# Kernel optimization log

Measured on AMD Instinct MI355X. Metric: run time of the kernel, lower is better.

The kernel has to match this reference:

```python
import jax, jax.numpy as jnp
import numpy as np

B, N, D, H = 4, 4096, 1024, 16
HD = D // H


def setup_inputs() -> dict:
    key = jax.random.key(0)
    k_x, k_qkv, k_proj, k_b = jax.random.split(key, 4)
    x = jax.random.normal(k_x, (B, N, D), dtype=jnp.float32)
    # torch nn.Linear weights: (out_features, in_features)
    w_qkv = jax.random.normal(k_qkv, (3 * D, D), dtype=jnp.float32) * (D ** -0.5)
    w_proj = jax.random.normal(k_proj, (D, D), dtype=jnp.float32) * (D ** -0.5)
    b_proj = jax.random.normal(k_b, (D,), dtype=jnp.float32) * 0.01
    return {"x": x, "w_qkv": w_qkv, "w_proj": w_proj, "b_proj": b_proj}


def reference(x, w_qkv, w_proj, b_proj):
    b, n, d = x.shape
    # qkv projection (no bias, qkv_bias=False)
    qkv = x @ w_qkv.T                       # (b, n, 3d)
    qkv = qkv.reshape(b, n, 3, H, HD)
    q, k, v = qkv[:, :, 0], qkv[:, :, 1], qkv[:, :, 2]   # each (b, n, H, HD)
    # Faithful to source: q @ k.transpose(-2,-1) with q,k of shape (b,n,H,HD)
    # -> per-token (H,H) attention across heads, softmax over last (head) axis.
    scale = HD ** -0.5
    attn = jnp.einsum('bnhd,bngd->bnhg', q, k) * scale   # (b, n, H, H)
    attn = jax.nn.softmax(attn, axis=-1)
    o = jnp.einsum('bnhg,bngd->bnhd', attn, v)           # (b, n, H, HD)
    # source: transpose(1,2).reshape(b,n,d) (contiguous copy then reshape)
    o = jnp.swapaxes(o, 1, 2).reshape(b, n, d)
    return o @ w_proj.T + b_proj
```

## Files before the change

### kernel.cpp

```cpp
#include <hip/hip_runtime.h>
#include <hip/hip_bf16.h>
#include <cstdint>
#include <cstddef>

#define NB      4
#define NSEQ    4096
#define DM      1024
#define NTOK    16384
#define QKV_N   3072
#define TPW     8

typedef __attribute__((ext_vector_type(8))) short short8_t;
typedef __attribute__((ext_vector_type(4))) short short4_t;
typedef __attribute__((ext_vector_type(4))) float f32x4;

static __device__ __forceinline__ unsigned short f2bf(float f) {
    unsigned u = __builtin_bit_cast(unsigned, f);
    u += 0x7fffu + ((u >> 16) & 1u);
    return (unsigned short)(u >> 16);
}

static __device__ __forceinline__ void async16(const void* g, void* l) {
    __builtin_amdgcn_global_load_lds(
        (const __attribute__((address_space(1))) void*)g,
        (__attribute__((address_space(3))) void*)l, 16, 0, 0);
}

__global__ void cvt_all(const float* __restrict__ x,
                        const float* __restrict__ wqkv,
                        const float* __restrict__ wproj,
                        unsigned short* __restrict__ xb,
                        unsigned short* __restrict__ wqkvb,
                        unsigned short* __restrict__ wprojb)
{
    const int stride = gridDim.x * blockDim.x;
    for (int i = blockIdx.x * blockDim.x + threadIdx.x; i < 5242880; i += stride) {
        const float* src; unsigned short* dst; int off;
        if (i < 4194304)      { src = x;     dst = xb;     off = i; }
        else if (i < 4980736) { src = wqkv;  dst = wqkvb;  off = i - 4194304; }
        else                  { src = wproj; dst = wprojb; off = i - 4980736; }
        float4 f = ((const float4*)src)[off];
        unsigned lo = (unsigned)f2bf(f.x) | ((unsigned)f2bf(f.y) << 16);
        unsigned hi = (unsigned)f2bf(f.z) | ((unsigned)f2bf(f.w) << 16);
        ((uint2*)dst)[off] = make_uint2(lo, hi);
    }
}

template <bool BF16_OUT, bool BIAS>
__global__ __launch_bounds__(512, 2)
void gemm256(const unsigned short* __restrict__ A,
             const unsigned short* __restrict__ Bm,
             void* __restrict__ Cv,
             const float* __restrict__ bias,
             int M, int N, int K)
{
    __shared__ alignas(16) unsigned short As[2][16384];
    __shared__ alignas(16) unsigned short Bs[2][16384];

    const int t    = threadIdx.x;
    const int lane = t & 63;
    const int wave = t >> 6;
    const int quad = lane >> 4;
    const int r16  = lane & 15;
    const int wm   = wave >> 2;
    const int wn   = wave & 3;

    const int nwg = gridDim.x;
    const int swz = (blockIdx.x & 7) * (nwg >> 3) + (blockIdx.x >> 3);
    const int ntn = N >> 8;
    const int tm  = swz / ntn, tn = swz - tm * ntn;
    const int m0  = tm << 8, n0 = tn << 8;

    const int srow = t >> 3;
    const int schk = ((t & 7) ^ (srow & 7)) << 3;
    const unsigned short* gA = A  + (size_t)(m0 + srow) * K + schk;
    const unsigned short* gB = Bm + (size_t)(n0 + srow) * K + schk;
    unsigned short* const lA = &As[0][0] + t * 8;
    unsigned short* const lB = &Bs[0][0] + t * 8;

    const int NT = K >> 6;

#define STA(buf, kt, r) async16(gA + (size_t)(r) * 64 * K + (size_t)(kt) * 64, \
                                lA + (buf) * 16384 + (r) * 4096)
#define STB(buf, kt, r) async16(gB + (size_t)(r) * 64 * K + (size_t)(kt) * 64, \
                                lB + (buf) * 16384 + (r) * 4096)

    const int cs0 = ((quad    ) ^ (r16 & 7)) << 3;
    const int cs1 = ((quad ^ 4) ^ (r16 & 7)) << 3;
    const int aRow = wm * 128 + r16;
    const int bRow = wn * 64  + r16;

    f32x4 acc[8][4] = {};

#define RD_A(QR) _Pragma("unroll") for (int ii = 0; ii < 4; ++ii) {            \
        a[ii][0] = *(const short8_t*)(Ab + (aRow + (QR)*64 + ii*16) * 64 + cs0); \
        a[ii][1] = *(const short8_t*)(Ab + (aRow + (QR)*64 + ii*16) * 64 + cs1); }
#define RD_B(bb, QC) _Pragma("unroll") for (int jj = 0; jj < 2; ++jj) {        \
        bb[jj][0] = *(const short8_t*)(Bb + (bRow + (QC)*32 + jj*16) * 64 + cs0); \
        bb[jj][1] = *(const short8_t*)(Bb + (bRow + (QC)*32 + jj*16) * 64 + cs1); }
#define MM(QR, QC, bb) _Pragma("unroll") for (int s = 0; s < 2; ++s)           \
      _Pragma("unroll") for (int ii = 0; ii < 4; ++ii)                          \
        _Pragma("unroll") for (int jj = 0; jj < 2; ++jj)                        \
          acc[(QR)*4+ii][(QC)*2+jj] = __builtin_amdgcn_mfma_f32_16x16x32_bf16( \
              a[ii][s], bb[jj][s], acc[(QR)*4+ii][(QC)*2+jj], 0, 0, 0);
#define SYNC_PRE  __builtin_amdgcn_s_barrier();                                \
                  asm volatile("s_waitcnt lgkmcnt(0)" ::: "memory");           \
                  __builtin_amdgcn_sched_barrier(0);                           \
                  __builtin_amdgcn_s_setprio(1);
#define SYNC_POST __builtin_amdgcn_s_setprio(0);                               \
                  __builtin_amdgcn_s_barrier();                                \
                  asm volatile("" ::: "memory");

    STA(0,0,0); STA(0,0,1); STA(0,0,2); STA(0,0,3);
    STB(0,0,0); STB(0,0,1); STB(0,0,2); STB(0,0,3);
    STA(1,1,0); STA(1,1,1); STA(1,1,2); STA(1,1,3);
    STB(1,1,0); STB(1,1,1); STB(1,1,2); STB(1,1,3);
    asm volatile("s_waitcnt vmcnt(8)" ::: "memory");
    __builtin_amdgcn_s_barrier();

    for (int g = 0; g < NT; ++g) {
        const int cur = g & 1;
        const unsigned short* Ab = &As[cur][0];
        const unsigned short* Bb = &Bs[cur][0];
        const bool pf = (g + 2 < NT);
        short8_t a[4][2], b0[2][2], b1[2][2];

        RD_A(0) RD_B(b0, 0)
        SYNC_PRE
        MM(0, 0, b0)
        SYNC_POST

        RD_B(b1, 1)
        if (pf) { STA(cur, g+2, 0); STA(cur, g+2, 2); }
        SYNC_PRE
        MM(0, 1, b1)
        SYNC_POST

        RD_A(1)
        if (pf) { STB(cur, g+2, 0); STB(cur, g+2, 1); }
        SYNC_PRE
        MM(1, 0, b0)
        SYNC_POST

        if (pf) { STA(cur, g+2, 1); STA(cur, g+2, 3);
                  STB(cur, g+2, 2); STB(cur, g+2, 3); }
        __builtin_amdgcn_s_barrier();
        __builtin_amdgcn_s_setprio(1);
        MM(1, 1, b1)
        __builtin_amdgcn_s_setprio(0);
        if (pf)              asm volatile("s_waitcnt vmcnt(8)" ::: "memory");
        else if (g + 1 < NT) asm volatile("s_waitcnt vmcnt(0)" ::: "memory");
        __builtin_amdgcn_s_barrier();
        asm volatile("" ::: "memory");
    }

#undef STA
#undef STB
#undef RD_A
#undef RD_B
#undef MM
#undef SYNC_PRE
#undef SYNC_POST

    #pragma unroll
    for (int ri = 0; ri < 8; ++ri) {
        const int row = m0 + wm * 128 + (ri >> 2) * 64 + (ri & 3) * 16 + quad * 4;
        #pragma unroll
        for (int cj = 0; cj < 4; ++cj) {
            const int col = n0 + wn * 64 + (cj >> 1) * 32 + (cj & 1) * 16 + r16;
            float bv = 0.f;
            if constexpr (BIAS) bv = bias[col];
            #pragma unroll
            for (int r = 0; r < 4; ++r) {
                float v = acc[ri][cj][r] + bv;
                if constexpr (BF16_OUT)
                    ((unsigned short*)Cv)[(size_t)(row + r) * N + col] = f2bf(v);
                else
                    ((float*)Cv)[(size_t)(row + r) * N + col] = v;
            }
        }
    }
}

__global__ __launch_bounds__(256)
void attn_kernel(const unsigned short* __restrict__ qkv,
                 unsigned short* __restrict__ operm)
{
    __shared__ alignas(16) unsigned short s_qkv[4][2][QKV_N];
    __shared__ alignas(16) unsigned short s_p[4][256];
    __shared__ alignas(16) unsigned short s_o[4][16 * 72];
    const int t     = threadIdx.x;
    const int lane  = t & 63;
    const int wave  = t >> 6;
    const int quad  = lane >> 4;
    const int r16   = lane & 15;
    const int tok0  = blockIdx.x * (4 * TPW) + wave * TPW;

    {
        const unsigned short* src = qkv + (size_t)tok0 * QKV_N;
        #pragma unroll
        for (int i = 0; i < 6; ++i)
            async16(src + i * 512 + lane * 8, &s_qkv[wave][0][i * 512 + lane * 8]);
    }

    #pragma unroll
    for (int it = 0; it < TPW; ++it) {
        const int buf   = it & 1;
        const int token = tok0 + it;

        if (it + 1 < TPW) {
            const unsigned short* src = qkv + (size_t)(token + 1) * QKV_N;
            #pragma unroll
            for (int i = 0; i < 6; ++i)
                async16(src + i * 512 + lane * 8,
                        &s_qkv[wave][buf ^ 1][i * 512 + lane * 8]);
        }
        if (it == 0)           { asm volatile("s_waitcnt vmcnt(6)" ::: "memory"); }
        else if (it + 1 < TPW) { asm volatile("s_waitcnt vmcnt(8)" ::: "memory"); }
        else                   { asm volatile("s_waitcnt vmcnt(2)" ::: "memory"); }
        __builtin_amdgcn_sched_barrier(0);

        const unsigned short* q  = &s_qkv[wave][buf][0];
        const unsigned short* kk = q + 1024;
        const unsigned short* vv = q + 2048;

        f32x4 s = {};
        #pragma unroll
        for (int c = 0; c < 64; c += 32) {
            short8_t aq = *(const short8_t*)(q  + r16 * 64 + c + quad * 8);
            short8_t bk = *(const short8_t*)(kk + r16 * 64 + c + quad * 8);
            s = __builtin_amdgcn_mfma_f32_16x16x32_bf16(aq, bk, s, 0, 0, 0);
        }

        #pragma unroll
        for (int r = 0; r < 4; ++r) {
            float x = s[r] * 0.125f;
            float m = x;
            #pragma unroll
            for (int o = 1; o < 16; o <<= 1) m = fmaxf(m, __shfl_xor(m, o));
            float e = __expf(x - m);
            float su = e;
            #pragma unroll
            for (int o = 1; o < 16; o <<= 1) su += __shfl_xor(su, o);
            s_p[wave][(quad * 4 + r) * 16 + r16] = f2bf(e * __builtin_amdgcn_rcpf(su));
        }

        f32x4 o[4];
#if __has_builtin(__builtin_amdgcn_mfma_f32_16x16x16bf16_1k)
        short4_t pa = *(const short4_t*)(&s_p[wave][r16 * 16 + quad * 4]);
        #pragma unroll
        for (int j = 0; j < 4; ++j) {
            short4_t vb;
            #pragma unroll
            for (int e = 0; e < 4; ++e)
                vb[e] = (short)vv[(quad * 4 + e) * 64 + j * 16 + r16];
            f32x4 z = {};
            o[j] = __builtin_amdgcn_mfma_f32_16x16x16bf16_1k(pa, vb, z, 0, 0, 0);
        }
#else
        short8_t pa = {};
        if (quad < 2) pa = *(const short8_t*)(&s_p[wave][r16 * 16 + quad * 8]);
        #pragma unroll
        for (int j = 0; j < 4; ++j) {
            short8_t vb = {};
            if (quad < 2) {
                #pragma unroll
                for (int e = 0; e < 8; ++e)
                    vb[e] = (short)vv[(quad * 8 + e) * 64 + j * 16 + r16];
            }
            f32x4 z = {};
            o[j] = __builtin_amdgcn_mfma_f32_16x16x32_bf16(pa, vb, z, 0, 0, 0);
        }
#endif

        #pragma unroll
        for (int j = 0; j < 4; ++j)
            #pragma unroll
            for (int r = 0; r < 4; ++r)
                s_o[wave][(quad * 4 + r) * 72 + j * 16 + r16] = f2bf(o[j][r]);

        const int b    = token >> 12;
        const int npos = token & 4095;
        const size_t base = (size_t)b * (NSEQ * DM)
                          + (size_t)(npos >> 4) * 1024
                          + (size_t)(npos & 15) * 64;
        #pragma unroll
        for (int c = lane; c < 128; c += 64) {
            const int h = c >> 3, part = c & 7;
            int4 val = *(const int4*)(&s_o[wave][h * 72 + part * 8]);
            *(int4*)(operm + base + (size_t)h * (256 * 1024) + part * 8) = val;
        }
    }
}

extern "C" void kernel_launch(void* const* d_in, const int* in_sizes, int n_in,
                              void* d_out, int out_size, void* d_ws, size_t ws_size,
                              hipStream_t stream)
{
    const float* x      = (const float*)d_in[0];
    const float* w_qkv  = (const float*)d_in[1];
    const float* w_proj = (const float*)d_in[2];
    const float* b_proj = (const float*)d_in[3];
    float* out = (float*)d_out;

    unsigned short* xb     = (unsigned short*)d_ws;
    unsigned short* wqkvb  = xb     + (size_t)16777216;
    unsigned short* wprojb = wqkvb  + (size_t)3145728;
    unsigned short* qkvb   = wprojb + (size_t)1048576;
    unsigned short* opermb = qkvb   + (size_t)50331648;

    cvt_all<<<2048, 256, 0, stream>>>(x, w_qkv, w_proj, xb, wqkvb, wprojb);

    gemm256<true, false><<<768, 512, 0, stream>>>(xb, wqkvb, qkvb, nullptr,
                                                  NTOK, QKV_N, DM);

    attn_kernel<<<NTOK / (4 * TPW), 256, 0, stream>>>(qkvb, opermb);

    gemm256<false, true><<<256, 512, 0, stream>>>(opermb, wprojb, out, b_proj,
                                                  NTOK, DM, DM);
}
```

Before: 305.9 us.

## Make QKV GEMM persistent with three tiles per block and cross-tile prefetch

The QKV GEMM is launched with 256 blocks, and each block now processes three 256x256 output tiles in sequence instead of launching 768 one-tile blocks. The K-loop spans all tiles, so prefetches for the next tile's first k-slices are issued while the current tile finishes, and the epilogue is written inside the loop before the accumulators are reset. This targets the wave-tail effect and the per-tile pipeline ramp-up and drain. In exchange, the epilogue stores now sit in the main loop and can stall the next tile, and the hardcoded 16 k-steps per tile assumes K=1024.

```diff
diff --git a/kernel.cpp b/kernel.cpp
--- a/kernel.cpp
+++ b/kernel.cpp
@@ -46,13 +46,13 @@
     }
 }
 
-template <bool BF16_OUT, bool BIAS>
-__global__ __launch_bounds__(512, 2)
-void gemm256(const unsigned short* __restrict__ A,
-             const unsigned short* __restrict__ Bm,
-             void* __restrict__ Cv,
-             const float* __restrict__ bias,
-             int M, int N, int K)
+template <bool BF16_OUT, bool BIAS, int TILES>
+__device__ __forceinline__
+void gemm256_body(const unsigned short* __restrict__ A,
+                  const unsigned short* __restrict__ Bm,
+                  void* __restrict__ Cv,
+                  const float* __restrict__ bias,
+                  int M, int N, int K)
 {
     __shared__ alignas(16) unsigned short As[2][16384];
     __shared__ alignas(16) unsigned short Bs[2][16384];
@@ -65,25 +65,30 @@
     const int wm   = wave >> 2;
     const int wn   = wave & 3;
 
-    const int nwg = gridDim.x;
-    const int swz = (blockIdx.x & 7) * (nwg >> 3) + (blockIdx.x >> 3);
     const int ntn = N >> 8;
-    const int tm  = swz / ntn, tn = swz - tm * ntn;
-    const int m0  = tm << 8, n0 = tn << 8;
+    const int cpx = (TILES * (int)gridDim.x) >> 3;
+    int m0c, n0c;
+    {
+        const int tid = blockIdx.x;
+        const int swz = (tid & 7) * cpx + (tid >> 3);
+        const int tm  = swz / ntn;
+        m0c = tm << 8;
+        n0c = (swz - tm * ntn) << 8;
+    }
 
     const int srow = t >> 3;
     const int schk = ((t & 7) ^ (srow & 7)) << 3;
-    const unsigned short* gA = A  + (size_t)(m0 + srow) * K + schk;
-    const unsigned short* gB = Bm + (size_t)(n0 + srow) * K + schk;
+    const unsigned short* pA = A  + (size_t)(m0c + srow) * K + schk;
+    const unsigned short* pB = Bm + (size_t)(n0c + srow) * K + schk;
     unsigned short* const lA = &As[0][0] + t * 8;
     unsigned short* const lB = &Bs[0][0] + t * 8;
 
-    const int NT = K >> 6;
-
-#define STA(buf, kt, r) async16(gA + (size_t)(r) * 64 * K + (size_t)(kt) * 64, \
-                                lA + (buf) * 16384 + (r) * 4096)
-#define STB(buf, kt, r) async16(gB + (size_t)(r) * 64 * K + (size_t)(kt) * 64, \
-                                lB + (buf) * 16384 + (r) * 4096)
+    const int NTtot = TILES << 4;
+
+#define STA(buf, kts, r) async16(pA + (size_t)(r) * 64 * K + (size_t)(kts) * 64, \
+                                 lA + (buf) * 16384 + (r) * 4096)
+#define STB(buf, kts, r) async16(pB + (size_t)(r) * 64 * K + (size_t)(kts) * 64, \
+                                 lB + (buf) * 16384 + (r) * 4096)
 
     const int cs0 = ((quad    ) ^ (r16 & 7)) << 3;
     const int cs1 = ((quad ^ 4) ^ (r16 & 7)) << 3;
@@ -118,11 +123,25 @@
     asm volatile("s_waitcnt vmcnt(8)" ::: "memory");
     __builtin_amdgcn_s_barrier();
 
-    for (int g = 0; g < NT; ++g) {
+    for (int g = 0; g < NTtot; ++g) {
         const int cur = g & 1;
         const unsigned short* Ab = &As[cur][0];
         const unsigned short* Bb = &Bs[cur][0];
-        const bool pf = (g + 2 < NT);
+        const bool pf = (g + 2 < NTtot);
+
+        if constexpr (TILES > 1) {
+            if (((g + 2) & 15) == 0) {
+                const int sj = (g + 2) >> 4;
+                if (sj < TILES) {
+                    const int tid = blockIdx.x + sj * (int)gridDim.x;
+                    const int swz = (tid & 7) * cpx + (tid >> 3);
+                    const int tm  = swz / ntn;
+                    pA = A  + (size_t)((tm << 8) + srow) * K + schk;
+                    pB = Bm + (size_t)(((swz - tm * ntn) << 8) + srow) * K + schk;
+                }
+            }
+        }
+        const int kts = (g + 2) & 15;
         short8_t a[4][2], b0[2][2], b1[2][2];
 
         RD_A(0) RD_B(b0, 0)
@@ -131,27 +150,62 @@
         SYNC_POST
 
         RD_B(b1, 1)
-        if (pf) { STA(cur, g+2, 0); STA(cur, g+2, 2); }
+        if (pf) { STA(cur, kts, 0); STA(cur, kts, 2); }
         SYNC_PRE
         MM(0, 1, b1)
         SYNC_POST
 
         RD_A(1)
-        if (pf) { STB(cur, g+2, 0); STB(cur, g+2, 1); }
+        if (pf) { STB(cur, kts, 0); STB(cur, kts, 1); }
         SYNC_PRE
         MM(1, 0, b0)
         SYNC_POST
 
-        if (pf) { STA(cur, g+2, 1); STA(cur, g+2, 3);
-                  STB(cur, g+2, 2); STB(cur, g+2, 3); }
+        if (pf) { STA(cur, kts, 1); STA(cur, kts, 3);
+                  STB(cur, kts, 2); STB(cur, kts, 3); }
         __builtin_amdgcn_s_barrier();
         __builtin_amdgcn_s_setprio(1);
         MM(1, 1, b1)
         __builtin_amdgcn_s_setprio(0);
-        if (pf)              asm volatile("s_waitcnt vmcnt(8)" ::: "memory");
-        else if (g + 1 < NT) asm volatile("s_waitcnt vmcnt(0)" ::: "memory");
+        if (pf)                 asm volatile("s_waitcnt vmcnt(8)" ::: "memory");
+        else if (g + 1 < NTtot) asm volatile("s_waitcnt vmcnt(0)" ::: "memory");
         __builtin_amdgcn_s_barrier();
         asm volatile("" ::: "memory");
+
+        if ((g & 15) == 15) {
+            #pragma unroll
+            for (int ri = 0; ri < 8; ++ri) {
+                const int row = m0c + wm * 128 + (ri >> 2) * 64 + (ri & 3) * 16 + quad * 4;
+                #pragma unroll
+                for (int cj = 0; cj < 4; ++cj) {
+                    const int col = n0c + wn * 64 + (cj >> 1) * 32 + (cj & 1) * 16 + r16;
+                    float bv = 0.f;
+                    if constexpr (BIAS) bv = bias[col];
+                    #pragma unroll
+                    for (int r = 0; r < 4; ++r) {
+                        float v = acc[ri][cj][r] + bv;
+                        if constexpr (BF16_OUT)
+                            ((unsigned short*)Cv)[(size_t)(row + r) * N + col] = f2bf(v);
+                        else
+                            ((float*)Cv)[(size_t)(row + r) * N + col] = v;
+                    }
+                }
+            }
+            if constexpr (TILES > 1) {
+                #pragma unroll
+                for (int ri = 0; ri < 8; ++ri)
+                    #pragma unroll
+                    for (int cj = 0; cj < 4; ++cj)
+                        acc[ri][cj] = (f32x4){0.f, 0.f, 0.f, 0.f};
+                if (g + 1 < NTtot) {
+                    const int tid = blockIdx.x + ((g + 1) >> 4) * (int)gridDim.x;
+                    const int swz = (tid & 7) * cpx + (tid >> 3);
+                    const int tm  = swz / ntn;
+                    m0c = tm << 8;
+                    n0c = (swz - tm * ntn) << 8;
+                }
+            }
+        }
     }
 
 #undef STA
@@ -161,25 +215,26 @@
 #undef MM
 #undef SYNC_PRE
 #undef SYNC_POST
-
-    #pragma unroll
-    for (int ri = 0; ri < 8; ++ri) {
-        const int row = m0 + wm * 128 + (ri >> 2) * 64 + (ri & 3) * 16 + quad * 4;
-        #pragma unroll
-        for (int cj = 0; cj < 4; ++cj) {
-            const int col = n0 + wn * 64 + (cj >> 1) * 32 + (cj & 1) * 16 + r16;
-            float bv = 0.f;
-            if constexpr (BIAS) bv = bias[col];
-            #pragma unroll
-            for (int r = 0; r < 4; ++r) {
-                float v = acc[ri][cj][r] + bv;
-                if constexpr (BF16_OUT)
-                    ((unsigned short*)Cv)[(size_t)(row + r) * N + col] = f2bf(v);
-                else
-                    ((float*)Cv)[(size_t)(row + r) * N + col] = v;
-            }
-        }
-    }
+}
+
+__global__ __launch_bounds__(512, 2)
+void gemm_qkv(const unsigned short* __restrict__ A,
+              const unsigned short* __restrict__ Bm,
+              void* __restrict__ Cv,
+              const float* __restrict__ bias,
+              int M, int N, int K)
+{
+    gemm256_body<true, false, 3>(A, Bm, Cv, bias, M, N, K);
+}
+
+__global__ __launch_bounds__(512, 2)
+void gemm_proj(const unsigned short* __restrict__ A,
+               const unsigned short* __restrict__ Bm,
+               void* __restrict__ Cv,
+               const float* __restrict__ bias,
+               int M, int N, int K)
+{
+    gemm256_body<false, true, 1>(A, Bm, Cv, bias, M, N, K);
 }
 
 __global__ __launch_bounds__(256)
@@ -311,11 +366,11 @@
 
     cvt_all<<<2048, 256, 0, stream>>>(x, w_qkv, w_proj, xb, wqkvb, wprojb);
 
-    gemm256<true, false><<<768, 512, 0, stream>>>(xb, wqkvb, qkvb, nullptr,
-                                                  NTOK, QKV_N, DM);
+    gemm_qkv<<<256, 512, 0, stream>>>(xb, wqkvb, qkvb, nullptr,
+                                      NTOK, QKV_N, DM);
 
     attn_kernel<<<NTOK / (4 * TPW), 256, 0, stream>>>(qkvb, opermb);
 
-    gemm256<false, true><<<256, 512, 0, stream>>>(opermb, wprojb, out, b_proj,
-                                                  NTOK, DM, DM);
-}
+    gemm_proj<<<256, 512, 0, stream>>>(opermb, wprojb, out, b_proj,
+                                       NTOK, DM, DM);
+}
```

New measurement: 307.5 us. About the same (+0.5%).
